# Performance work log

Measured on AMD Instinct MI355X. Metric: run time of the kernel, lower is better.

## Reference

```python
import jax, jax.numpy as jnp
import numpy as np

EPS = 1e-8  # F.cosine_similarity default eps


def setup_inputs() -> dict:
    key = jax.random.key(0)
    k1, k2, k3, k4 = jax.random.split(key, 4)
    Q, P, E, V = 4096, 16384, 128, 30000
    query = jax.random.randint(k1, (Q,), 0, V, dtype=jnp.int64)
    para = jax.random.randint(k2, (P,), 0, V, dtype=jnp.int64)
    que_embed = jax.random.normal(k3, (Q, E), dtype=jnp.float32)
    para_embed = jax.random.normal(k4, (P, E), dtype=jnp.float32)
    return {"query": query, "para": para, "que_embed": que_embed, "para_embed": para_embed}


def reference(query, para, que_embed, para_embed):
    # xor_matrix[i, j] = 1 if query[i] == para[j] else 0  -> [Q, P] int64
    xor_matrix = (query[:, None] == para[None, :]).astype(jnp.int64)
    # cos_matrix[i, j] = cosine_similarity(que_embed[i], para_embed[j])
    # torch semantics: dot / (max(||q||, eps) * max(||p||, eps))
    q_norm = jnp.maximum(jnp.linalg.norm(que_embed, axis=-1), EPS)   # [Q]
    p_norm = jnp.maximum(jnp.linalg.norm(para_embed, axis=-1), EPS)  # [P]
    dots = jnp.einsum('qe,pe->qp', que_embed, para_embed)            # [Q, P]
    cos_matrix = dots / (q_norm[:, None] * p_norm[None, :])
    return xor_matrix, cos_matrix
```

## Files before the change

kernel.cpp:

```cpp
#include <hip/hip_runtime.h>
#include <stdint.h>

typedef __attribute__((ext_vector_type(8))) short bf16x8;
typedef __attribute__((ext_vector_type(4))) float f32x4;

__device__ __forceinline__ uint32_t f2bf(float f) {
    uint32_t u = __builtin_bit_cast(uint32_t, f);
    u += 0x7fffu + ((u >> 16) & 1u);
    return u >> 16;
}
__device__ __forceinline__ uint32_t pack2(float a, float b) {
    return f2bf(a) | (f2bf(b) << 16);
}

__global__ __launch_bounds__(256) void prep_norms(const float* __restrict__ qe,
                                                  const float* __restrict__ pe,
                                                  float* __restrict__ rq,
                                                  float* __restrict__ rp,
                                                  int Q, int Pn) {
    int gw = (blockIdx.x * 256 + threadIdx.x) >> 6;
    int lane = threadIdx.x & 63;
    if (gw >= Q + Pn) return;
    const float* src = (gw < Q) ? (qe + (size_t)gw * 128) : (pe + (size_t)(gw - Q) * 128);
    float2 v = *(const float2*)(src + lane * 2);
    float s = v.x * v.x + v.y * v.y;
#pragma unroll
    for (int off = 32; off > 0; off >>= 1) s += __shfl_down(s, off, 64);
    if (lane == 0) {
        float r = 1.0f / fmaxf(sqrtf(s), 1e-8f);
        if (gw < Q) rq[gw] = r; else rp[gw - Q] = r;
    }
}

__global__ __launch_bounds__(256) void conv_frag(const float* __restrict__ src,
                                                 unsigned short* __restrict__ dst,
                                                 int ngroups) {
    int t = blockIdx.x * 256 + threadIdx.x;
    if (t >= ngroups * 256) return;
    int g = t >> 8, rem = t & 255;
    int c = rem >> 6, lane = rem & 63;
    int row = g * 16 + (lane & 15);
    int col = c * 32 + ((lane >> 4) << 3);
    const float* s = src + (size_t)row * 128 + col;
    float4 a0 = *(const float4*)s;
    float4 a1 = *(const float4*)(s + 4);
    uint4 pk = { pack2(a0.x, a0.y), pack2(a0.z, a0.w),
                 pack2(a1.x, a1.y), pack2(a1.z, a1.w) };
    *(uint4*)(dst + (size_t)t * 8) = pk;
}

#define PBLK   2048
#define PFLUSH 256

__global__ __launch_bounds__(256, 4) void fused_gemm(
        const unsigned short* __restrict__ Qf, const unsigned short* __restrict__ Pf,
        const int* __restrict__ qid, const int* __restrict__ pid,
        const float* __restrict__ rq, const float* __restrict__ rp,
        float* __restrict__ oxor, float* __restrict__ ocos, int Pn) {
    __shared__ __align__(16) float scos[16 * 260];

    const int nwg = gridDim.x;
    const int chunk = nwg >> 3;
    const int bid = blockIdx.x;
    const int wg = (bid & 7) * chunk + (bid >> 3);
    const int nPc = Pn / PBLK;
    const int qg = wg / nPc;
    const int pc = wg % nPc;
    const int pblock = pc * PBLK;

    const int t = threadIdx.x;
    const int lane = t & 63;
    const int w = t >> 6;
    const int lq = lane & 15;
    const int g4 = (lane >> 4) << 2;

    bf16x8 af[4];
    const unsigned short* abase = Qf + ((size_t)(qg * 4) * 64 + lane) * 8;
#pragma unroll
    for (int kk = 0; kk < 4; ++kk)
        af[kk] = *(const bf16x8*)(abase + kk * 512);

    const int qrow_base = qg * 16;
    const float rqv = rq[qrow_base + lq];

    for (int fl = 0; fl < PBLK / PFLUSH; ++fl) {
        const int fbase = pblock + fl * PFLUSH;
#pragma unroll
        for (int f = 0; f < 4; ++f) {
            const int cidx = f * 4 + w;
            const int p0 = fbase + cidx * 16;
            const unsigned short* bbase = Pf + ((size_t)(p0 >> 4) * 4) * 512 + (size_t)lane * 8;
            bf16x8 bfr[4];
#pragma unroll
            for (int kk = 0; kk < 4; ++kk)
                bfr[kk] = *(const bf16x8*)(bbase + kk * 512);
            f32x4 acc = {0.f, 0.f, 0.f, 0.f};
#pragma unroll
            for (int kk = 0; kk < 4; ++kk)
                acc = __builtin_amdgcn_mfma_f32_16x16x32_bf16(bfr[kk], af[kk], acc, 0, 0, 0);
            const float4 rpv = *(const float4*)(rp + p0 + g4);
            f32x4 c4 = { acc[0]*rqv*rpv.x, acc[1]*rqv*rpv.y,
                         acc[2]*rqv*rpv.z, acc[3]*rqv*rpv.w };
            *(f32x4*)&scos[lq * 260 + cidx * 16 + g4] = c4;
        }
        __syncthreads();
        const int4 pv4 = *(const int4*)(pid + fbase + lane * 4);
#pragma unroll
        for (int r = 0; r < 4; ++r) {
            const int row = w * 4 + r;
            const int qvr = qid[qrow_base + row];
            const size_t obase = (size_t)(qrow_base + row) * Pn + fbase;
            f32x4 vc = *(const f32x4*)&scos[row * 260 + lane * 4];
            f32x4 vx = { qvr==pv4.x?1.f:0.f, qvr==pv4.y?1.f:0.f,
                         qvr==pv4.z?1.f:0.f, qvr==pv4.w?1.f:0.f };
            __builtin_nontemporal_store(vc, (f32x4*)(ocos + obase + lane * 4));
            __builtin_nontemporal_store(vx, (f32x4*)(oxor + obase + lane * 4));
        }
        __syncthreads();
    }
}

extern "C" void kernel_launch(void* const* d_in, const int* in_sizes, int n_in,
                              void* d_out, int out_size, void* d_ws, size_t ws_size,
                              hipStream_t stream) {
    const int*   qid = (const int*)d_in[0];
    const int*   pid = (const int*)d_in[1];
    const float* qe  = (const float*)d_in[2];
    const float* pe  = (const float*)d_in[3];
    const int Q  = in_sizes[0];
    const int Pn = in_sizes[1];

    unsigned short* Qf = (unsigned short*)d_ws;
    unsigned short* Pf = Qf + (size_t)Q * 128;
    float* rq = (float*)(Pf + (size_t)Pn * 128);
    float* rp = rq + Q;

    float* oxor = (float*)d_out;
    float* ocos = oxor + (size_t)Q * (size_t)Pn;

    const int qgroups = Q / 16, pgroups = Pn / 16;
    conv_frag<<<qgroups, 256, 0, stream>>>(qe, Qf, qgroups);
    conv_frag<<<pgroups, 256, 0, stream>>>(pe, Pf, pgroups);
    prep_norms<<<(Q + Pn + 3) / 4, 256, 0, stream>>>(qe, pe, rq, rp, Q, Pn);

    const int nblocks = (Q / 16) * (Pn / PBLK);
    fused_gemm<<<nblocks, 256, 0, stream>>>(Qf, Pf, qid, pid, rq, rp, oxor, ocos, Pn);
}
```

Baseline: 138.8 us.

## Use per-wave LDS staging to drop block barriers in fused GEMM epilogue

Each wave now owns a private 16x64 LDS tile covering 64 contiguous P columns, so the block-wide __syncthreads around the staging buffer are removed. The epilogue writes 16 rows with scalar 4-byte nontemporal stores per lane (256 B per row per wave) instead of 4 rows of 16-byte vector stores across 256 columns. The goal is to remove barrier stalls and let waves proceed independently. In exchange, stores are narrower and more numerous, which may reduce write efficiency on this output-bandwidth-bound kernel. The padded stride of 65 is meant to avoid LDS bank conflicts.

```diff
diff --git a/kernel.cpp b/kernel.cpp
--- a/kernel.cpp
+++ b/kernel.cpp
@@ -49,15 +49,14 @@
     *(uint4*)(dst + (size_t)t * 8) = pk;
 }
 
-#define PBLK   2048
-#define PFLUSH 256
+#define PBLK 2048
 
 __global__ __launch_bounds__(256, 4) void fused_gemm(
         const unsigned short* __restrict__ Qf, const unsigned short* __restrict__ Pf,
         const int* __restrict__ qid, const int* __restrict__ pid,
         const float* __restrict__ rq, const float* __restrict__ rp,
         float* __restrict__ oxor, float* __restrict__ ocos, int Pn) {
-    __shared__ __align__(16) float scos[16 * 260];
+    __shared__ __align__(16) float scos[4 * 16 * 65];
 
     const int nwg = gridDim.x;
     const int chunk = nwg >> 3;
@@ -73,6 +72,7 @@
     const int w = t >> 6;
     const int lq = lane & 15;
     const int g4 = (lane >> 4) << 2;
+    const int wbase = w * (16 * 65);
 
     bf16x8 af[4];
     const unsigned short* abase = Qf + ((size_t)(qg * 4) * 64 + lane) * 8;
@@ -83,13 +83,12 @@
     const int qrow_base = qg * 16;
     const float rqv = rq[qrow_base + lq];
 
-    for (int fl = 0; fl < PBLK / PFLUSH; ++fl) {
-        const int fbase = pblock + fl * PFLUSH;
+    for (int fl = 0; fl < PBLK / 256; ++fl) {
+        const int pw = pblock + fl * 256 + w * 64;
 #pragma unroll
         for (int f = 0; f < 4; ++f) {
-            const int cidx = f * 4 + w;
-            const int p0 = fbase + cidx * 16;
-            const unsigned short* bbase = Pf + ((size_t)(p0 >> 4) * 4) * 512 + (size_t)lane * 8;
+            const int p0 = pw + f * 16;
+            const unsigned short* bbase = Pf + (size_t)(p0 >> 4) * 2048 + (size_t)lane * 8;
             bf16x8 bfr[4];
 #pragma unroll
             for (int kk = 0; kk < 4; ++kk)
@@ -99,24 +98,22 @@
             for (int kk = 0; kk < 4; ++kk)
                 acc = __builtin_amdgcn_mfma_f32_16x16x32_bf16(bfr[kk], af[kk], acc, 0, 0, 0);
             const float4 rpv = *(const float4*)(rp + p0 + g4);
-            f32x4 c4 = { acc[0]*rqv*rpv.x, acc[1]*rqv*rpv.y,
-                         acc[2]*rqv*rpv.z, acc[3]*rqv*rpv.w };
-            *(f32x4*)&scos[lq * 260 + cidx * 16 + g4] = c4;
+            const int a0 = wbase + lq * 65 + f * 16 + g4;
+            scos[a0 + 0] = acc[0] * rqv * rpv.x;
+            scos[a0 + 1] = acc[1] * rqv * rpv.y;
+            scos[a0 + 2] = acc[2] * rqv * rpv.z;
+            scos[a0 + 3] = acc[3] * rqv * rpv.w;
         }
-        __syncthreads();
-        const int4 pv4 = *(const int4*)(pid + fbase + lane * 4);
+        const int pvl = pid[pw + lane];
 #pragma unroll
-        for (int r = 0; r < 4; ++r) {
-            const int row = w * 4 + r;
-            const int qvr = qid[qrow_base + row];
-            const size_t obase = (size_t)(qrow_base + row) * Pn + fbase;
-            f32x4 vc = *(const f32x4*)&scos[row * 260 + lane * 4];
-            f32x4 vx = { qvr==pv4.x?1.f:0.f, qvr==pv4.y?1.f:0.f,
-                         qvr==pv4.z?1.f:0.f, qvr==pv4.w?1.f:0.f };
-            __builtin_nontemporal_store(vc, (f32x4*)(ocos + obase + lane * 4));
-            __builtin_nontemporal_store(vx, (f32x4*)(oxor + obase + lane * 4));
+        for (int r = 0; r < 16; ++r) {
+            const int qvr = qid[qrow_base + r];
+            const size_t obase = (size_t)(qrow_base + r) * Pn + pw;
+            float vc = scos[wbase + r * 65 + lane];
+            float vx = (qvr == pvl) ? 1.f : 0.f;
+            __builtin_nontemporal_store(vc, ocos + obase + lane);
+            __builtin_nontemporal_store(vx, oxor + obase + lane);
         }
-        __syncthreads();
     }
 }
 
```

Result: faster. 132.3 us (-4.7%).
